# Optimization experiments

Measured on AMD Instinct MI355X. Metric: run time of the kernel, lower is better.

Reference implementation:

```python
import jax, jax.numpy as jnp
import numpy as np

B, T, D, H = 1, 2048, 1024, 16
Dh = D // H
GSA_SCALE = 0.25
LN_EPS = 1e-5


def setup_inputs() -> dict:
    key = jax.random.key(0)
    ks = jax.random.split(key, 24)
    s = 0.02
    def W(k, din, dout):
        return jax.random.normal(k, (din, dout), jnp.float32) * s
    inp = dict(
        x=jax.random.normal(ks[0], (B, T, D), jnp.float32),
        mask=jnp.ones((B, T, T), jnp.bool_),
        # MultiHeadAttention params (linears[0..3] = q,k,v,o)
        mha_wq=W(ks[1], D, D), mha_bq=jnp.zeros((D,), jnp.float32),
        mha_wk=W(ks[2], D, D), mha_bk=jnp.zeros((D,), jnp.float32),
        mha_wv=W(ks[3], D, D), mha_bv=jnp.zeros((D,), jnp.float32),
        mha_wo=W(ks[4], D, D), mha_bo=jnp.zeros((D,), jnp.float32),
        # _GeodesicSelfAttention params
        gsa_wq=W(ks[5], D, D), gsa_bq=jnp.zeros((D,), jnp.float32),
        gsa_wk=W(ks[6], D, D), gsa_bk=jnp.zeros((D,), jnp.float32),
        gsa_wv=W(ks[7], D, D), gsa_bv=jnp.zeros((D,), jnp.float32),
        gsa_wo=W(ks[8], D, D), gsa_bo=jnp.zeros((D,), jnp.float32),
        log_diag=jnp.zeros((H, Dh), jnp.float32),  # nn.Parameter(torch.zeros(h, dk))
        # LayerNorms
        ln_mha_g=jnp.ones((D,), jnp.float32), ln_mha_b=jnp.zeros((D,), jnp.float32),
        ln_gsa_g=jnp.ones((D,), jnp.float32), ln_gsa_b=jnp.zeros((D,), jnp.float32),
        # mix scalar (initialized to -2.0 in __init__)
        gsa_mix=jnp.asarray(-2.0, jnp.float32),
        # gate: Linear(D,D) -> GELU -> Linear(D,1), last bias filled with 0.5
        gate_w1=W(ks[9], D, D), gate_b1=jnp.zeros((D,), jnp.float32),
        gate_w2=W(ks[10], D, 1), gate_b2=jnp.full((1,), 0.5, jnp.float32),
    )
    return inp


def _ln(x, g, b):
    m = x.mean(-1, keepdims=True)
    v = ((x - m) ** 2).mean(-1, keepdims=True)
    return (x - m) / jnp.sqrt(v + LN_EPS) * g + b


def _heads(y):  # [B,T,D] -> [B,H,T,Dh]
    return y.reshape(B, T, H, Dh).transpose(0, 2, 1, 3)


def _merge(y):  # [B,H,T,Dh] -> [B,T,D]
    return y.transpose(0, 2, 1, 3).reshape(B, T, D)


def _forward(x, mask, mha_wq, mha_bq, mha_wk, mha_bk, mha_wv, mha_bv, mha_wo, mha_bo,
             gsa_wq, gsa_bq, gsa_wk, gsa_bk, gsa_wv, gsa_bv, gsa_wo, gsa_bo,
             log_diag, ln_mha_g, ln_mha_b, ln_gsa_g, ln_gsa_b, gsa_mix,
             gate_w1, gate_b1, gate_w2, gate_b2):
    inv_sqrt_dh = 1.0 / jnp.sqrt(jnp.float32(Dh))
    m4 = mask[:, None, :, :]  # [B,1,T,T]

    # ---- standard MHA branch ----
    q = _heads(x @ mha_wq + mha_bq)
    k = _heads(x @ mha_wk + mha_bk)
    v = _heads(x @ mha_wv + mha_bv)
    scores = jnp.einsum('bhtd,bhsd->bhts', q, k) * inv_sqrt_dh
    scores = jnp.where(m4, scores, -jnp.inf)
    p = jax.nn.softmax(scores, axis=-1)
    mha_out = _merge(jnp.einsum('bhts,bhsd->bhtd', p, v)) @ mha_wo + mha_bo

    # ---- geodesic (Mahalanobis) branch ----
    qg = _heads(x @ gsa_wq + gsa_bq)
    kg = _heads(x @ gsa_wk + gsa_bk)
    vg = _heads(x @ gsa_wv + gsa_bv)
    diag = jax.nn.softplus(log_diag) + 1e-6          # [H,Dh]
    diag4 = diag[None, :, None, :]
    qM = qg * diag4
    q2M = (qg * qM).sum(-1)                           # [B,H,T]
    k2M = (kg * (kg * diag4)).sum(-1)                 # [B,H,T]
    cross = jnp.einsum('bhtd,bhsd->bhts', qM, kg)     # [B,H,T,T]
    dist = q2M[..., :, None] + k2M[..., None, :] - 2.0 * cross
    s = -0.5 * dist * inv_sqrt_dh
    s = jnp.where(m4, s, -jnp.inf)
    all_inf = jnp.all(jnp.isneginf(s), axis=-1, keepdims=True)
    s = jnp.where(all_inf, 0.0, s)
    pg = jax.nn.softmax(s * GSA_SCALE, axis=-1)
    gsa_out = _merge(jnp.einsum('bhts,bhsd->bhtd', pg, vg)) @ gsa_wo + gsa_bo

    # ---- gated mix ----
    mha_out = _ln(mha_out, ln_mha_g, ln_mha_b)
    gsa_out = jax.nn.sigmoid(gsa_mix) * _ln(gsa_out, ln_gsa_g, ln_gsa_b)
    g = jax.nn.gelu(x @ gate_w1 + gate_b1, approximate=False) @ gate_w2 + gate_b2
    alpha = 0.9 * jax.nn.sigmoid(g)                   # alpha_cap = 0.9, [B,T,1]
    return alpha * mha_out + (1.0 - alpha) * gsa_out


def reference(x, mask, mha_wq, mha_bq, mha_wk, mha_bk, mha_wv, mha_bv, mha_wo, mha_bo,
              gsa_wq, gsa_bq, gsa_wk, gsa_bk, gsa_wv, gsa_bv, gsa_wo, gsa_bo,
              log_diag, ln_mha_g, ln_mha_b, ln_gsa_g, ln_gsa_b, gsa_mix,
              gate_w1, gate_b1, gate_w2, gate_b2):
    return _forward(x, mask, mha_wq, mha_bq, mha_wk, mha_bk, mha_wv, mha_bv, mha_wo, mha_bo,
                    gsa_wq, gsa_bq, gsa_wk, gsa_bk, gsa_wv, gsa_bv, gsa_wo, gsa_bo,
                    log_diag, ln_mha_g, ln_mha_b, ln_gsa_g, ln_gsa_b, gsa_mix,
                    gate_w1, gate_b1, gate_w2, gate_b2)
```

## Files before the change

### kernel.cpp

```cpp
#include <hip/hip_runtime.h>
#include <stdint.h>

typedef unsigned short u16;
typedef u16   u16x4  __attribute__((ext_vector_type(4)));
typedef u16   u16x8  __attribute__((ext_vector_type(8)));
typedef __bf16 bf16x8 __attribute__((ext_vector_type(8)));
typedef float f32x4  __attribute__((ext_vector_type(4)));

#define SEQ   2048
#define DM    1024
#define NHEAD 16
#define DHEAD 64

#define QM_SCALE 0.180336880f
#define QG_SCALE 0.045084220f
#define K2_SCALE 0.022542110f

static __device__ __forceinline__ u16 f2b(float f) {
  uint32_t u = __float_as_uint(f);
  u += 0x7fffu + ((u >> 16) & 1u);
  return (u16)(u >> 16);
}
static __device__ __forceinline__ float b2f(u16 u) {
  return __uint_as_float(((uint32_t)u) << 16);
}

static __device__ __forceinline__ void gload16(const u16* g, u16* l) {
  __builtin_amdgcn_global_load_lds(
      (const __attribute__((address_space(1))) unsigned int*)g,
      (__attribute__((address_space(3))) unsigned int*)l, 16, 0, 0);
}

struct PrepArgs { const float* w[9]; u16* o[9];
                  const float* x; u16* xb; const float* log_diag; float* diag; };

__global__ __launch_bounds__(256) void prep_kernel(PrepArgs a) {
  const int z = blockIdx.z, tid = threadIdx.x;
  if (z == 9) {
    int b = blockIdx.y * 16 + blockIdx.x;
#pragma unroll
    for (int j = 0; j < 8; ++j) {
      int idx = b * 8192 + j * 1024 + tid * 4;
      float4 v = *(const float4*)&a.x[idx];
      u16x4 w = {f2b(v.x), f2b(v.y), f2b(v.z), f2b(v.w)};
      *(u16x4*)&a.xb[idx] = w;
    }
    if (b == 0) {
#pragma unroll
      for (int j = 0; j < 4; ++j) {
        int i = j * 256 + tid;
        float v = a.log_diag[i];
        float sp = (v > 20.f) ? v : log1pf(__expf(v));
        a.diag[i] = sp + 1e-6f;
      }
    }
    return;
  }
  const float* __restrict__ src = a.w[z];
  u16* __restrict__ dst = a.o[z];
  int r0 = blockIdx.y * 64, c0 = blockIdx.x * 64;
  __shared__ float tile[64][65];
  int r = tid >> 2, o8 = (tid & 3) * 16;
#pragma unroll
  for (int i = 0; i < 16; i += 4) {
    float4 v = *(const float4*)&src[(r0 + r) * DM + c0 + o8 + i];
    tile[r][o8 + i + 0] = v.x; tile[r][o8 + i + 1] = v.y;
    tile[r][o8 + i + 2] = v.z; tile[r][o8 + i + 3] = v.w;
  }
  __syncthreads();
  u16x8 w0, w1;
#pragma unroll
  for (int i = 0; i < 8; ++i) w0[i] = f2b(tile[o8 + i][r]);
#pragma unroll
  for (int i = 0; i < 8; ++i) w1[i] = f2b(tile[o8 + 8 + i][r]);
  *(u16x8*)&dst[(c0 + r) * DM + r0 + o8]     = w0;
  *(u16x8*)&dst[(c0 + r) * DM + r0 + o8 + 8] = w1;
}

struct GemmDesc { const u16* A; const u16* Bt; const float* bias; void* out;
                  float* aux; int mode; int k0; int klen; float scale; };
struct GemmParams { GemmDesc d[8]; const float* diag; };

__global__ __launch_bounds__(256) void gemm_bt_kernel(GemmParams p) {
  GemmDesc g = p.d[blockIdx.z];
  const int K = DM;
  const int m0 = blockIdx.y * 128, n0 = blockIdx.x * 64;
  const int tid = threadIdx.x;
  const int wave = tid >> 6, lane = tid & 63, ln = lane & 15, quad = lane >> 4;

  __shared__ __align__(16) u16 As[2 * 128 * 32];
  __shared__ __align__(16) u16 Bs[2 * 64 * 32];

  const f32x4 fz = {0.f, 0.f, 0.f, 0.f};
  f32x4 acc[2][4];
#pragma unroll
  for (int i = 0; i < 2; ++i)
#pragma unroll
    for (int j = 0; j < 4; ++j) acc[i][j] = fz;

  const u16* Aps[4]; const u16* Bps[2];
#pragma unroll
  for (int s = 0; s < 4; ++s) {
    int vr = s * 64 + (tid >> 2);
    Aps[s] = g.A + (size_t)(m0 + (vr & 127)) * K + g.k0 + (vr >> 7) * 32 + (tid & 3) * 8;
  }
#pragma unroll
  for (int s = 0; s < 2; ++s) {
    int vr = s * 64 + (tid >> 2);
    Bps[s] = g.Bt + (size_t)(n0 + (vr & 63)) * K + g.k0 + (vr >> 6) * 32 + (tid & 3) * 8;
  }

  for (int kk = 0; kk < g.klen; kk += 64) {
#pragma unroll
    for (int s = 0; s < 4; ++s) gload16(Aps[s] + kk, &As[s * 2048 + tid * 8]);
#pragma unroll
    for (int s = 0; s < 2; ++s) gload16(Bps[s] + kk, &Bs[s * 2048 + tid * 8]);
    __syncthreads();
#pragma unroll
    for (int c = 0; c < 2; ++c) {
      bf16x8 af[2], bfr[4];
#pragma unroll
      for (int mb = 0; mb < 2; ++mb)
        af[mb] = *(const bf16x8*)&As[(c * 128 + wave * 32 + mb * 16 + ln) * 32 + quad * 8];
#pragma unroll
      for (int nb = 0; nb < 4; ++nb)
        bfr[nb] = *(const bf16x8*)&Bs[(c * 64 + nb * 16 + ln) * 32 + quad * 8];
#pragma unroll
      for (int mb = 0; mb < 2; ++mb)
#pragma unroll
        for (int nb = 0; nb < 4; ++nb)
          acc[mb][nb] = __builtin_amdgcn_mfma_f32_16x16x32_bf16(af[mb], bfr[nb], acc[mb][nb], 0, 0, 0);
    }
    __syncthreads();
  }

  const int mode = g.mode;
  const int h = n0 >> 6;
#pragma unroll
  for (int mb = 0; mb < 2; ++mb) {
    int row = m0 + wave * 32 + mb * 16 + quad * 4;
    float ksum[4] = {0.f, 0.f, 0.f, 0.f};
#pragma unroll
    for (int nb = 0; nb < 4; ++nb) {
      int col = n0 + nb * 16 + ln;
      float bv = g.bias ? g.bias[col] : 0.f;
      f32x4 a = acc[mb][nb];
      if (mode == 5) {
        u16x4 w;
#pragma unroll
        for (int r = 0; r < 4; ++r) w[r] = f2b(a[r] + bv);
        *(u16x4*)&((u16*)g.out)[((size_t)(h * 64) + nb * 16 + ln) * SEQ + row] = w;
        continue;
      }
#pragma unroll
      for (int r = 0; r < 4; ++r) {
        float v = a[r] + bv;
        int rw = row + r;
        if (mode == 0) {
          ((u16*)g.out)[((size_t)h * SEQ + rw) * DHEAD + (col & 63)] = f2b(v);
        } else if (mode == 1) {
          ((u16*)g.out)[((size_t)h * SEQ + rw) * DHEAD + (col & 63)] = f2b(v * g.scale);
        } else if (mode == 2) {
          ((u16*)g.out)[((size_t)h * SEQ + rw) * DHEAD + (col & 63)] = f2b(v * p.diag[col] * g.scale);
        } else if (mode == 3) {
          float gg = 0.5f * v * (1.f + erff(v * 0.70710678f));
          ((u16*)g.out)[(size_t)rw * DM + col] = f2b(gg);
        } else if (mode == 4) {
          ((float*)g.out)[(size_t)rw * DM + col] = v;
        } else {
          ((u16*)g.out)[((size_t)h * SEQ + rw) * DHEAD + (col & 63)] = f2b(v);
          ksum[r] += v * v * p.diag[col];
        }
      }
    }
    if (mode == 6) {
#pragma unroll
      for (int r = 0; r < 4; ++r) {
        float s = ksum[r];
        s += __shfl_xor(s, 1); s += __shfl_xor(s, 2);
        s += __shfl_xor(s, 4); s += __shfl_xor(s, 8);
        if (ln == 0) g.aux[(size_t)h * SEQ + row + r] = s * K2_SCALE;
      }
    }
  }
}

__global__ __launch_bounds__(256) void flash_kernel(
    const u16* __restrict__ Qm, const u16* __restrict__ Km, const u16* __restrict__ VmT,
    const u16* __restrict__ Qg, const u16* __restrict__ Kg, const u16* __restrict__ VgT,
    const float* __restrict__ k2m, u16* __restrict__ attM, u16* __restrict__ attG) {
  const int z = blockIdx.z;
  const u16* __restrict__ Q  = z ? Qg  : Qm;
  const u16* __restrict__ Kp = z ? Kg  : Km;
  const u16* __restrict__ Vt = z ? VgT : VmT;
  u16* __restrict__ out = z ? attG : attM;
  const int h = blockIdx.y;
  const int tid = threadIdx.x, wave = tid >> 6, lane = tid & 63, ln = lane & 15, quad = lane >> 4;
  const int wrow = blockIdx.x * 64 + wave * 16;

  __shared__ __align__(16) u16 Ks[64 * 72];
  __shared__ __align__(16) u16 Vs[80 * 72];
  __shared__ __align__(16) u16 Pt[4][16 * 72];
  __shared__ float k2s[64];

  bf16x8 qf[2];
#pragma unroll
  for (int kb = 0; kb < 2; ++kb)
    qf[kb] = *(const bf16x8*)&Q[((size_t)(h * SEQ) + wrow + ln) * 64 + kb * 32 + quad * 8];

  const f32x4 fz = {0.f, 0.f, 0.f, 0.f};
  f32x4 o[5];
#pragma unroll
  for (int db = 0; db < 5; ++db) o[db] = fz;

  const int sr = tid >> 2, sc = (tid & 3) * 16;
  const u16* Kbase = Kp + (size_t)h * SEQ * 64;
  const u16* Vbase = Vt + (size_t)h * 64 * SEQ;

  if (tid < 36) ((uint32_t*)&Vs[64 * 72])[tid] = 0x3F803F80u;

  u16x8 kr0 = *(const u16x8*)&Kbase[(size_t)sr * 64 + sc];
  u16x8 kr1 = *(const u16x8*)&Kbase[(size_t)sr * 64 + sc + 8];
  u16x8 vr0 = *(const u16x8*)&Vbase[(size_t)sr * SEQ + sc];
  u16x8 vr1 = *(const u16x8*)&Vbase[(size_t)sr * SEQ + sc + 8];
  float k2r = 0.f;
  if (z && tid < 64) k2r = k2m[h * SEQ + tid];

  for (int kt = 0; kt < SEQ; kt += 64) {
    *(u16x8*)&Ks[sr * 72 + sc]     = kr0;
    *(u16x8*)&Ks[sr * 72 + sc + 8] = kr1;
    *(u16x8*)&Vs[sr * 72 + sc]     = vr0;
    *(u16x8*)&Vs[sr * 72 + sc + 8] = vr1;
    if (z && tid < 64) k2s[tid] = k2r;
    __syncthreads();
    if (kt + 64 < SEQ) {
      kr0 = *(const u16x8*)&Kbase[(size_t)(kt + 64 + sr) * 64 + sc];
      kr1 = *(const u16x8*)&Kbase[(size_t)(kt + 64 + sr) * 64 + sc + 8];
      vr0 = *(const u16x8*)&Vbase[(size_t)sr * SEQ + kt + 64 + sc];
      vr1 = *(const u16x8*)&Vbase[(size_t)sr * SEQ + kt + 64 + sc + 8];
      if (z && tid < 64) k2r = k2m[h * SEQ + kt + 64 + tid];
    }

    f32x4 st[4];
#pragma unroll
    for (int sb = 0; sb < 4; ++sb) {
      st[sb] = fz;
      bf16x8 kf0 = *(const bf16x8*)&Ks[(sb * 16 + ln) * 72 + quad * 8];
      bf16x8 kf1 = *(const bf16x8*)&Ks[(sb * 16 + ln) * 72 + 32 + quad * 8];
      st[sb] = __builtin_amdgcn_mfma_f32_16x16x32_bf16(kf0, qf[0], st[sb], 0, 0, 0);
      st[sb] = __builtin_amdgcn_mfma_f32_16x16x32_bf16(kf1, qf[1], st[sb], 0, 0, 0);
    }

#pragma unroll
    for (int sb = 0; sb < 4; ++sb) {
      if (z) {
        f32x4 b4 = *(const f32x4*)&k2s[sb * 16 + quad * 4];
#pragma unroll
        for (int r = 0; r < 4; ++r) st[sb][r] -= b4[r];
      }
      uint32_t eb[4];
#pragma unroll
      for (int r = 0; r < 4; ++r)
        eb[r] = __float_as_uint(__builtin_amdgcn_exp2f(st[sb][r]));
      uint32_t lo = __builtin_amdgcn_perm(eb[1], eb[0], 0x07060302u);
      uint32_t hi = __builtin_amdgcn_perm(eb[3], eb[2], 0x07060302u);
      uint2 pk = {lo, hi};
      *(uint2*)&Pt[wave][ln * 72 + sb * 16 + quad * 4] = pk;
    }
    __asm__ __volatile__("" ::: "memory");

    bf16x8 pf0 = *(const bf16x8*)&Pt[wave][ln * 72 + quad * 8];
    bf16x8 pf1 = *(const bf16x8*)&Pt[wave][ln * 72 + 32 + quad * 8];
#pragma unroll
    for (int db = 0; db < 5; ++db) {
      bf16x8 vf0 = *(const bf16x8*)&Vs[(db * 16 + ln) * 72 + quad * 8];
      bf16x8 vf1 = *(const bf16x8*)&Vs[(db * 16 + ln) * 72 + 32 + quad * 8];
      o[db] = __builtin_amdgcn_mfma_f32_16x16x32_bf16(vf0, pf0, o[db], 0, 0, 0);
      o[db] = __builtin_amdgcn_mfma_f32_16x16x32_bf16(vf1, pf1, o[db], 0, 0, 0);
    }
    __syncthreads();
  }

  float l_all = __shfl(o[4][0], ln);
  float inv = 1.f / l_all;
#pragma unroll
  for (int db = 0; db < 4; ++db) {
    u16x4 w;
#pragma unroll
    for (int r = 0; r < 4; ++r) w[r] = f2b(o[db][r] * inv);
    *(u16x4*)&out[(size_t)(wrow + ln) * DM + h * 64 + db * 16 + quad * 4] = w;
  }
}

__global__ __launch_bounds__(256) void final_kernel(
    const float* __restrict__ p0, const float* __restrict__ p1,
    const float* __restrict__ p2, const float* __restrict__ p3,
    const u16* __restrict__ G1, const float* __restrict__ w2,
    const float* __restrict__ b2, const float* __restrict__ mixp,
    const float* __restrict__ gm, const float* __restrict__ bm,
    const float* __restrict__ gg, const float* __restrict__ bg,
    float* __restrict__ out) {
  int t = blockIdx.x, tid = threadIdx.x;
  float xm[4], xg[4];
  float sm = 0.f, sm2 = 0.f, sg = 0.f, sg2 = 0.f, sd = 0.f;
#pragma unroll
  for (int j0 = 0; j0 < 4; ++j0) {
    int j = tid + j0 * 256;
    size_t idx = (size_t)t * DM + j;
    float a = p0[idx] + p1[idx];
    float b = p2[idx] + p3[idx];
    xm[j0] = a; xg[j0] = b;
    sm += a; sm2 += a * a; sg += b; sg2 += b * b;
    sd += b2f(G1[idx]) * w2[j];
  }
#pragma unroll
  for (int d = 32; d >= 1; d >>= 1) {
    sm += __shfl_xor(sm, d); sm2 += __shfl_xor(sm2, d);
    sg += __shfl_xor(sg, d); sg2 += __shfl_xor(sg2, d);
    sd += __shfl_xor(sd, d);
  }
  __shared__ float red[5][4];
  int wave = tid >> 6;
  if ((tid & 63) == 0) {
    red[0][wave] = sm; red[1][wave] = sm2; red[2][wave] = sg;
    red[3][wave] = sg2; red[4][wave] = sd;
  }
  __syncthreads();
  sm  = red[0][0] + red[0][1] + red[0][2] + red[0][3];
  sm2 = red[1][0] + red[1][1] + red[1][2] + red[1][3];
  sg  = red[2][0] + red[2][1] + red[2][2] + red[2][3];
  sg2 = red[3][0] + red[3][1] + red[3][2] + red[3][3];
  sd  = red[4][0] + red[4][1] + red[4][2] + red[4][3];

  float mm = sm / DM, vm = fmaxf(sm2 / DM - mm * mm, 0.f);
  float rm = rsqrtf(vm + 1e-5f);
  float mg = sg / DM, vg = fmaxf(sg2 / DM - mg * mg, 0.f);
  float rg = rsqrtf(vg + 1e-5f);
  float alpha = 0.9f / (1.f + __expf(-(sd + b2[0])));
  float mix = 1.f / (1.f + __expf(-mixp[0]));
#pragma unroll
  for (int j0 = 0; j0 < 4; ++j0) {
    int j = tid + j0 * 256;
    float lm = (xm[j0] - mm) * rm * gm[j] + bm[j];
    float lg = (xg[j0] - mg) * rg * gg[j] + bg[j];
    out[(size_t)t * DM + j] = alpha * lm + (1.f - alpha) * mix * lg;
  }
}

extern "C" void kernel_launch(void* const* d_in, const int* in_sizes, int n_in,
                              void* d_out, int out_size, void* d_ws, size_t ws_size,
                              hipStream_t stream) {
  const float* x        = (const float*)d_in[0];
  const float* mha_wq = (const float*)d_in[2];
  const float* mha_bq = (const float*)d_in[3];
  const float* mha_wk = (const float*)d_in[4];
  const float* mha_bk = (const float*)d_in[5];
  const float* mha_wv = (const float*)d_in[6];
  const float* mha_bv = (const float*)d_in[7];
  const float* mha_wo = (const float*)d_in[8];
  const float* mha_bo = (const float*)d_in[9];
  const float* gsa_wq = (const float*)d_in[10];
  const float* gsa_bq = (const float*)d_in[11];
  const float* gsa_wk = (const float*)d_in[12];
  const float* gsa_bk = (const float*)d_in[13];
  const float* gsa_wv = (const float*)d_in[14];
  const float* gsa_bv = (const float*)d_in[15];
  const float* gsa_wo = (const float*)d_in[16];
  const float* gsa_bo = (const float*)d_in[17];
  const float* log_diag = (const float*)d_in[18];
  const float* ln_mha_g = (const float*)d_in[19];
  const float* ln_mha_b = (const float*)d_in[20];
  const float* ln_gsa_g = (const float*)d_in[21];
  const float* ln_gsa_b = (const float*)d_in[22];
  const float* gsa_mix  = (const float*)d_in[23];
  const float* gate_w1  = (const float*)d_in[24];
  const float* gate_b1  = (const float*)d_in[25];
  const float* gate_w2  = (const float*)d_in[26];
  const float* gate_b2  = (const float*)d_in[27];

  char* ws = (char*)d_ws;
  size_t off = 0;
  auto alloc = [&](size_t bytes) -> void* {
    void* p = ws + off;
    off += (bytes + 255) & ~(size_t)255;
    return p;
  };

  u16* xb = (u16*)alloc((size_t)SEQ * DM * 2);
  u16* wT[9];
  for (int i = 0; i < 9; ++i) wT[i] = (u16*)alloc((size_t)DM * DM * 2);
  float* diag = (float*)alloc((size_t)DM * 4);
  u16* Qm  = (u16*)alloc((size_t)SEQ * DM * 2);
  u16* Km  = (u16*)alloc((size_t)SEQ * DM * 2);
  u16* Qg  = (u16*)alloc((size_t)SEQ * DM * 2);
  u16* Kg  = (u16*)alloc((size_t)SEQ * DM * 2);
  u16* VmT = (u16*)alloc((size_t)SEQ * DM * 2);
  u16* VgT = (u16*)alloc((size_t)SEQ * DM * 2);
  float* k2m = (float*)alloc((size_t)NHEAD * SEQ * 4);
  u16* G1   = (u16*)alloc((size_t)SEQ * DM * 2);
  u16* attM = (u16*)alloc((size_t)SEQ * DM * 2);
  u16* attG = (u16*)alloc((size_t)SEQ * DM * 2);
  float* proj3 = (float*)alloc((size_t)SEQ * DM * 4);
  float* proj0 = (float*)Qm;
  float* proj1 = (float*)Qg;
  float* proj2 = (float*)VmT;

  PrepArgs pa;
  pa.w[0] = mha_wq; pa.w[1] = mha_wk; pa.w[2] = mha_wv; pa.w[3] = mha_wo;
  pa.w[4] = gsa_wq; pa.w[5] = gsa_wk; pa.w[6] = gsa_wv; pa.w[7] = gsa_wo;
  pa.w[8] = gate_w1;
  for (int i = 0; i < 9; ++i) pa.o[i] = wT[i];
  pa.x = x; pa.xb = xb; pa.log_diag = log_diag; pa.diag = diag;
  prep_kernel<<<dim3(16, 16, 10), 256, 0, stream>>>(pa);

  GemmParams gp{};
  gp.diag = diag;
  gp.d[0] = {xb, wT[0], mha_bq, (void*)Qm,  nullptr, 1, 0, DM, QM_SCALE};
  gp.d[1] = {xb, wT[1], mha_bk, (void*)Km,  nullptr, 0, 0, DM, 1.f};
  gp.d[2] = {xb, wT[2], mha_bv, (void*)VmT, nullptr, 5, 0, DM, 1.f};
  gp.d[3] = {xb, wT[4], gsa_bq, (void*)Qg,  nullptr, 2, 0, DM, QG_SCALE};
  gp.d[4] = {xb, wT[5], gsa_bk, (void*)Kg,  k2m,     6, 0, DM, 1.f};
  gp.d[5] = {xb, wT[6], gsa_bv, (void*)VgT, nullptr, 5, 0, DM, 1.f};
  gp.d[6] = {xb, wT[8], gate_b1,(void*)G1,  nullptr, 3, 0, DM, 1.f};
  gemm_bt_kernel<<<dim3(16, 16, 7), 256, 0, stream>>>(gp);

  flash_kernel<<<dim3(SEQ / 64, NHEAD, 2), 256, 0, stream>>>(Qm, Km, VmT, Qg, Kg, VgT, k2m, attM, attG);

  GemmParams gp2{};
  gp2.diag = diag;
  gp2.d[0] = {attM, wT[3], mha_bo, (void*)proj0, nullptr, 4, 0,   512, 1.f};
  gp2.d[1] = {attM, wT[3], nullptr,(void*)proj1, nullptr, 4, 512, 512, 1.f};
  gp2.d[2] = {attG, wT[7], gsa_bo, (void*)proj2, nullptr, 4, 0,   512, 1.f};
  gp2.d[3] = {attG, wT[7], nullptr,(void*)proj3, nullptr, 4, 512, 512, 1.f};
  gemm_bt_kernel<<<dim3(16, 16, 4), 256, 0, stream>>>(gp2);

  final_kernel<<<SEQ, 256, 0, stream>>>(proj0, proj1, proj2, proj3, G1,
                                        gate_w2, gate_b2, gsa_mix,
                                        ln_mha_g, ln_mha_b, ln_gsa_g, ln_gsa_b,
                                        (float*)d_out);
}
```

Measured before the change: 299.9 us.

## Process two 16-row query blocks per wave in flash attention kernel

```diff
diff --git a/kernel.cpp b/kernel.cpp
--- a/kernel.cpp
+++ b/kernel.cpp
@@ -196,22 +196,26 @@
   u16* __restrict__ out = z ? attG : attM;
   const int h = blockIdx.y;
   const int tid = threadIdx.x, wave = tid >> 6, lane = tid & 63, ln = lane & 15, quad = lane >> 4;
-  const int wrow = blockIdx.x * 64 + wave * 16;
+  const int wrow = blockIdx.x * 128 + wave * 32;
 
   __shared__ __align__(16) u16 Ks[64 * 72];
   __shared__ __align__(16) u16 Vs[80 * 72];
-  __shared__ __align__(16) u16 Pt[4][16 * 72];
+  __shared__ __align__(16) u16 Pt[4][32 * 72];
   __shared__ float k2s[64];
 
-  bf16x8 qf[2];
-#pragma unroll
-  for (int kb = 0; kb < 2; ++kb)
-    qf[kb] = *(const bf16x8*)&Q[((size_t)(h * SEQ) + wrow + ln) * 64 + kb * 32 + quad * 8];
+  bf16x8 qf[2][2];
+#pragma unroll
+  for (int qb = 0; qb < 2; ++qb)
+#pragma unroll
+    for (int kb = 0; kb < 2; ++kb)
+      qf[qb][kb] = *(const bf16x8*)&Q[((size_t)(h * SEQ) + wrow + qb * 16 + ln) * 64 + kb * 32 + quad * 8];
 
   const f32x4 fz = {0.f, 0.f, 0.f, 0.f};
-  f32x4 o[5];
-#pragma unroll
-  for (int db = 0; db < 5; ++db) o[db] = fz;
+  f32x4 o[2][5];
+#pragma unroll
+  for (int qb = 0; qb < 2; ++qb)
+#pragma unroll
+    for (int db = 0; db < 5; ++db) o[qb][db] = fz;
 
   const int sr = tid >> 2, sc = (tid & 3) * 16;
   const u16* Kbase = Kp + (size_t)h * SEQ * 64;
@@ -241,54 +245,71 @@
       if (z && tid < 64) k2r = k2m[h * SEQ + kt + 64 + tid];
     }
 
-    f32x4 st[4];
+    bf16x8 kf0[4], kf1[4];
 #pragma unroll
     for (int sb = 0; sb < 4; ++sb) {
-      st[sb] = fz;
-      bf16x8 kf0 = *(const bf16x8*)&Ks[(sb * 16 + ln) * 72 + quad * 8];
-      bf16x8 kf1 = *(const bf16x8*)&Ks[(sb * 16 + ln) * 72 + 32 + quad * 8];
-      st[sb] = __builtin_amdgcn_mfma_f32_16x16x32_bf16(kf0, qf[0], st[sb], 0, 0, 0);
-      st[sb] = __builtin_amdgcn_mfma_f32_16x16x32_bf16(kf1, qf[1], st[sb], 0, 0, 0);
-    }
-
-#pragma unroll
-    for (int sb = 0; sb < 4; ++sb) {
-      if (z) {
-        f32x4 b4 = *(const f32x4*)&k2s[sb * 16 + quad * 4];
-#pragma unroll
-        for (int r = 0; r < 4; ++r) st[sb][r] -= b4[r];
-      }
-      uint32_t eb[4];
-#pragma unroll
-      for (int r = 0; r < 4; ++r)
-        eb[r] = __float_as_uint(__builtin_amdgcn_exp2f(st[sb][r]));
-      uint32_t lo = __builtin_amdgcn_perm(eb[1], eb[0], 0x07060302u);
-      uint32_t hi = __builtin_amdgcn_perm(eb[3], eb[2], 0x07060302u);
-      uint2 pk = {lo, hi};
-      *(uint2*)&Pt[wave][ln * 72 + sb * 16 + quad * 4] = pk;
+      kf0[sb] = *(const bf16x8*)&Ks[(sb * 16 + ln) * 72 + quad * 8];
+      kf1[sb] = *(const bf16x8*)&Ks[(sb * 16 + ln) * 72 + 32 + quad * 8];
+    }
+
+#pragma unroll
+    for (int qb = 0; qb < 2; ++qb) {
+      f32x4 st[4];
+#pragma unroll
+      for (int sb = 0; sb < 4; ++sb) {
+        st[sb] = fz;
+        st[sb] = __builtin_amdgcn_mfma_f32_16x16x32_bf16(kf0[sb], qf[qb][0], st[sb], 0, 0, 0);
+        st[sb] = __builtin_amdgcn_mfma_f32_16x16x32_bf16(kf1[sb], qf[qb][1], st[sb], 0, 0, 0);
+      }
+#pragma unroll
+      for (int sb = 0; sb < 4; ++sb) {
+        if (z) {
+          f32x4 b4 = *(const f32x4*)&k2s[sb * 16 + quad * 4];
+#pragma unroll
+          for (int r = 0; r < 4; ++r) st[sb][r] -= b4[r];
+        }
+        uint32_t eb[4];
+#pragma unroll
+        for (int r = 0; r < 4; ++r)
+          eb[r] = __float_as_uint(__builtin_amdgcn_exp2f(st[sb][r]));
+        uint32_t lo = __builtin_amdgcn_perm(eb[1], eb[0], 0x07060302u);
+        uint32_t hi = __builtin_amdgcn_perm(eb[3], eb[2], 0x07060302u);
+        uint2 pk = {lo, hi};
+        *(uint2*)&Pt[wave][(qb * 16 + ln) * 72 + sb * 16 + quad * 4] = pk;
+      }
     }
     __asm__ __volatile__("" ::: "memory");
 
-    bf16x8 pf0 = *(const bf16x8*)&Pt[wave][ln * 72 + quad * 8];
-    bf16x8 pf1 = *(const bf16x8*)&Pt[wave][ln * 72 + 32 + quad * 8];
+    bf16x8 pf[2][2];
+#pragma unroll
+    for (int qb = 0; qb < 2; ++qb) {
+      pf[qb][0] = *(const bf16x8*)&Pt[wave][(qb * 16 + ln) * 72 + quad * 8];
+      pf[qb][1] = *(const bf16x8*)&Pt[wave][(qb * 16 + ln) * 72 + 32 + quad * 8];
+    }
 #pragma unroll
     for (int db = 0; db < 5; ++db) {
       bf16x8 vf0 = *(const bf16x8*)&Vs[(db * 16 + ln) * 72 + quad * 8];
       bf16x8 vf1 = *(const bf16x8*)&Vs[(db * 16 + ln) * 72 + 32 + quad * 8];
-      o[db] = __builtin_amdgcn_mfma_f32_16x16x32_bf16(vf0, pf0, o[db], 0, 0, 0);
-      o[db] = __builtin_amdgcn_mfma_f32_16x16x32_bf16(vf1, pf1, o[db], 0, 0, 0);
+#pragma unroll
+      for (int qb = 0; qb < 2; ++qb) {
+        o[qb][db] = __builtin_amdgcn_mfma_f32_16x16x32_bf16(vf0, pf[qb][0], o[qb][db], 0, 0, 0);
+        o[qb][db] = __builtin_amdgcn_mfma_f32_16x16x32_bf16(vf1, pf[qb][1], o[qb][db], 0, 0, 0);
+      }
     }
     __syncthreads();
   }
 
-  float l_all = __shfl(o[4][0], ln);
-  float inv = 1.f / l_all;
-#pragma unroll
-  for (int db = 0; db < 4; ++db) {
-    u16x4 w;
-#pragma unroll
-    for (int r = 0; r < 4; ++r) w[r] = f2b(o[db][r] * inv);
-    *(u16x4*)&out[(size_t)(wrow + ln) * DM + h * 64 + db * 16 + quad * 4] = w;
+#pragma unroll
+  for (int qb = 0; qb < 2; ++qb) {
+    float l_all = __shfl(o[qb][4][0], ln);
+    float inv = 1.f / l_all;
+#pragma unroll
+    for (int db = 0; db < 4; ++db) {
+      u16x4 w;
+#pragma unroll
+      for (int r = 0; r < 4; ++r) w[r] = f2b(o[qb][db][r] * inv);
+      *(u16x4*)&out[(size_t)(wrow + qb * 16 + ln) * DM + h * 64 + db * 16 + quad * 4] = w;
+    }
   }
 }
 
@@ -424,7 +445,7 @@
   gp.d[6] = {xb, wT[8], gate_b1,(void*)G1,  nullptr, 3, 0, DM, 1.f};
   gemm_bt_kernel<<<dim3(16, 16, 7), 256, 0, stream>>>(gp);
 
-  flash_kernel<<<dim3(SEQ / 64, NHEAD, 2), 256, 0, stream>>>(Qm, Km, VmT, Qg, Kg, VgT, k2m, attM, attG);
+  flash_kernel<<<dim3(SEQ / 128, NHEAD, 2), 256, 0, stream>>>(Qm, Km, VmT, Qg, Kg, VgT, k2m, attM, attG);
 
   GemmParams gp2{};
   gp2.diag = diag;
```

New measurement: 291.8 us. 1.03x faster.
